# Kernel tuning notes

Measured on AMD Instinct MI355X. Metric: run time of the kernel, lower is better.

The kernel has to match this reference:

```python
import jax, jax.numpy as jnp
import numpy as np
import math

N, S, E, H = 4, 4096, 1024, 16
D = E // H  # head_dim = 64


def setup_inputs() -> dict:
    key = jax.random.key(0)
    ks = jax.random.split(key, 9)
    w = 1.0 / math.sqrt(E)
    mk = lambda k, shape: (jax.random.normal(k, shape, jnp.float32) * w)
    return {
        "x": jax.random.normal(ks[0], (N, S, E), jnp.float32),
        "Wq": mk(ks[1], (E, E)), "bq": mk(ks[2], (E,)),
        "Wk": mk(ks[3], (E, E)), "bk": mk(ks[4], (E,)),
        "Wv": mk(ks[5], (E, E)), "bv": mk(ks[6], (E,)),
        "Wo": mk(ks[7], (E, E)), "bo": mk(ks[8], (E,)),
    }


def reference(x, Wq, bq, Wk, bk, Wv, bv, Wo, bo):
    n, s, e = x.shape
    h, d = H, D
    scale = 1.0 / math.sqrt(d)

    def proj(W, b):
        # nn.Linear: x @ W.T + b, then view(N,S,H,D).transpose(1,2) -> (N,H,S,D)
        y = jnp.einsum('nse,fe->nsf', x, W) + b
        return y.reshape(n, s, h, d).transpose(0, 2, 1, 3)  # (N,H,S,D)

    Q = proj(Wq, bq)
    K = proj(Wk, bk)
    V = proj(Wv, bv)

    # Faithful reproduction of the source's einsum applied to ALREADY-transposed
    # (N,H,S,D) tensors: labels n,q,h,d bind to actual dims N,H,S,D, so the
    # result is (N, S, H, H) -- heads attending to heads at each position.
    scores = jnp.einsum('nqhd,nkhd->nhqk', Q, K) * scale  # (N,S,H,H)
    attn = jax.nn.softmax(scores, axis=-1)
    # Second einsum: attn labels n,h,q,l bind to N,S,H,H; V labels n,l,h,d bind
    # to N,H,S,D. Output nqhd has actual shape (N,H,S,D).
    out = jnp.einsum('nhql,nlhd->nqhd', attn, V)  # (N,H,S,D)
    out = out.reshape(n, s, e)  # scrambled flat reshape, as in the source
    return jnp.einsum('nse,fe->nsf', out, Wo) + bo
```

## Files before the change

kernel.cpp:

```cpp
#include <hip/hip_runtime.h>
#include <hip/hip_fp16.h>
#include <stddef.h>


typedef _Float16 f16_t;
typedef _Float16 f16x8 __attribute__((ext_vector_type(8)));
typedef _Float16 f16x4 __attribute__((ext_vector_type(4)));
typedef float    f32x4 __attribute__((ext_vector_type(4)));

static constexpr int Sdim = 4096;
static constexpr int Edim = 1024;
static constexpr int Mrows = 4 * Sdim;
static constexpr size_t MATEL = (size_t)Mrows * Edim;
static constexpr size_t WEL = (size_t)Edim * Edim;
static constexpr int BM = 128, BN = 128, BK = 32;
static constexpr int TILE = BM * BK;

__device__ __forceinline__ void gload_lds16(const f16_t* g, f16_t* l) {
  __builtin_amdgcn_global_load_lds(
      (const __attribute__((address_space(1))) void*)g,
      (__attribute__((address_space(3))) void*)l, 16, 0, 0);
}

__global__ __launch_bounds__(256) void cvt_kernel(
    const float* __restrict__ s0, const float* __restrict__ s1,
    const float* __restrict__ s2, const float* __restrict__ s3,
    const float* __restrict__ s4,
    f16_t* __restrict__ d0, f16_t* __restrict__ d1, f16_t* __restrict__ d2,
    f16_t* __restrict__ d3, f16_t* __restrict__ d4) {
  const float* s; f16_t* d; size_t nv;
  switch (blockIdx.y) {
    case 0: s = s0; d = d0; nv = MATEL / 4; break;
    case 1: s = s1; d = d1; nv = WEL / 4; break;
    case 2: s = s2; d = d2; nv = WEL / 4; break;
    case 3: s = s3; d = d3; nv = WEL / 4; break;
    default: s = s4; d = d4; nv = WEL / 4; break;
  }
  const size_t stride = (size_t)gridDim.x * 256;
  for (size_t i = blockIdx.x * 256 + threadIdx.x; i < nv; i += stride) {
    const f32x4 v = ((const f32x4*)s)[i];
    f16x4 h;
#pragma unroll
    for (int j = 0; j < 4; j++) h[j] = (f16_t)v[j];
    ((f16x4*)d)[i] = h;
  }
}

template <bool SCRA, typename TOut>
__device__ __forceinline__ void gemm_f16(const f16_t* __restrict__ A,
                                         const f16_t* __restrict__ B,
                                         const float* __restrict__ bias,
                                         TOut* __restrict__ C) {
  __shared__ __align__(16) f16_t As[TILE];
  __shared__ __align__(16) f16_t Bs[TILE];
  const int t = threadIdx.x;
  const int bm = blockIdx.x * BM;
  const int bn = blockIdx.y * BN;
  const int lane = t & 63;
  const int wave = t >> 6;
  const int wm = (wave >> 1) * 64;
  const int wn = (wave & 1) * 64;
  const int row16 = lane & 15;
  const int quad = lane >> 4;

  f32x4 acc[4][4] = {};

  const int lr = t >> 2;
  const int lc = (t & 3) * 8;
  f16_t* la = &As[t * 8];
  f16_t* lb = &Bs[t * 8];
  const f16_t* gb = B + (size_t)(bn + lr) * Edim + lc;

  for (int k0 = 0; k0 < Edim; k0 += BK) {
#pragma unroll
    for (int half = 0; half < 2; half++) {
      const f16_t* ga;
      if constexpr (SCRA) {
        const int R = bm + lr + half * 64;
        const int n = R >> 12, h = (R >> 8) & 15, shi = R & 255;
        const int c = k0 + lc;
        ga = A + ((size_t)((n << 12) + (shi << 4) + (c >> 6))) * Edim +
             (h << 6) + (c & 63);
      } else {
        ga = A + (size_t)(bm + lr + half * 64) * Edim + k0 + lc;
      }
      gload_lds16(ga, la + half * (64 * BK));
      gload_lds16(gb + k0 + half * (size_t)(64 * Edim), lb + half * (64 * BK));
    }
    __syncthreads();

    f16x8 af[4], bf[4];
#pragma unroll
    for (int i = 0; i < 4; i++)
      af[i] = *(const f16x8*)&As[(wm + i * 16 + row16) * BK + quad * 8];
#pragma unroll
    for (int j = 0; j < 4; j++)
      bf[j] = *(const f16x8*)&Bs[(wn + j * 16 + row16) * BK + quad * 8];
#pragma unroll
    for (int i = 0; i < 4; i++)
#pragma unroll
      for (int j = 0; j < 4; j++)
        acc[i][j] = __builtin_amdgcn_mfma_f32_16x16x32_f16(af[i], bf[j], acc[i][j], 0, 0, 0);
    __syncthreads();
  }

#pragma unroll
  for (int j = 0; j < 4; j++) {
    const int col = bn + wn + j * 16 + row16;
    const float bv = bias[col];
#pragma unroll
    for (int i = 0; i < 4; i++) {
      const int rb = bm + wm + i * 16 + quad * 4;
#pragma unroll
      for (int r = 0; r < 4; r++)
        C[(size_t)(rb + r) * Edim + col] = (TOut)(acc[i][j][r] + bv);
    }
  }
}

__global__ __launch_bounds__(256) void qkv_kernel(
    const f16_t* __restrict__ x,
    const f16_t* __restrict__ Wq, const float* __restrict__ bq,
    const f16_t* __restrict__ Wk, const float* __restrict__ bk,
    const f16_t* __restrict__ Wv, const float* __restrict__ bv,
    f16_t* __restrict__ Qb, f16_t* __restrict__ Kb, f16_t* __restrict__ Vb) {
  const f16_t* W; const float* bi; f16_t* C;
  if (blockIdx.z == 0)      { W = Wq; bi = bq; C = Qb; }
  else if (blockIdx.z == 1) { W = Wk; bi = bk; C = Kb; }
  else                      { W = Wv; bi = bv; C = Vb; }
  gemm_f16<false, f16_t>(x, W, bi, C);
}

__global__ __launch_bounds__(256) void outp_kernel(
    const f16_t* __restrict__ Ab, const f16_t* __restrict__ Wo,
    const float* __restrict__ bo, float* __restrict__ out) {
  gemm_f16<true, float>(Ab, Wo, bo, out);
}

__global__ __launch_bounds__(256) void attn_kernel(f16_t* __restrict__ Qb,
                                                   const f16_t* __restrict__ Kb,
                                                   const f16_t* __restrict__ Vb) {
  const int pos = blockIdx.x;
  __shared__ float q[16][65], k[16][65], v[16][65];
  __shared__ float p[16][17];
  const int t = threadIdx.x;
  f16_t* Qr = Qb + (size_t)pos * Edim;
  const f16_t* Kr = Kb + (size_t)pos * Edim;
  const f16_t* Vr = Vb + (size_t)pos * Edim;

  {
    const int h = t >> 4, d0 = (t & 15) * 4;
    const f16x4 qq = *(const f16x4*)(Qr + 4 * t);
    const f16x4 kk = *(const f16x4*)(Kr + 4 * t);
    const f16x4 vv = *(const f16x4*)(Vr + 4 * t);
#pragma unroll
    for (int j = 0; j < 4; j++) {
      q[h][d0 + j] = (float)qq[j];
      k[h][d0 + j] = (float)kk[j];
      v[h][d0 + j] = (float)vv[j];
    }
  }
  __syncthreads();
  {
    const int qh = t >> 4, kh = t & 15;
    float a = 0.f;
#pragma unroll
    for (int d = 0; d < 64; d++) a += q[qh][d] * k[kh][d];
    p[qh][kh] = a * 0.125f;
  }
  __syncthreads();
  if (t < 16) {
    float m = -1e30f;
#pragma unroll
    for (int kh = 0; kh < 16; kh++) m = fmaxf(m, p[t][kh]);
    float e[16], sum = 0.f;
#pragma unroll
    for (int kh = 0; kh < 16; kh++) { e[kh] = __expf(p[t][kh] - m); sum += e[kh]; }
    const float inv = 1.f / sum;
#pragma unroll
    for (int kh = 0; kh < 16; kh++) p[t][kh] = e[kh] * inv;
  }
  __syncthreads();
  {
    const int h = t >> 4, d0 = (t & 15) * 4;
    float o0 = 0.f, o1 = 0.f, o2 = 0.f, o3 = 0.f;
#pragma unroll
    for (int l = 0; l < 16; l++) {
      const float w = p[h][l];
      o0 += w * v[l][d0];
      o1 += w * v[l][d0 + 1];
      o2 += w * v[l][d0 + 2];
      o3 += w * v[l][d0 + 3];
    }
    f16x4 r;
    r[0] = (f16_t)o0; r[1] = (f16_t)o1; r[2] = (f16_t)o2; r[3] = (f16_t)o3;
    *(f16x4*)(Qr + 4 * t) = r;
  }
}

extern "C" void kernel_launch(void* const* d_in, const int* in_sizes, int n_in,
                              void* d_out, int out_size, void* d_ws, size_t ws_size,
                              hipStream_t stream) {
  const float* x  = (const float*)d_in[0];
  const float* Wq = (const float*)d_in[1];
  const float* bq = (const float*)d_in[2];
  const float* Wk = (const float*)d_in[3];
  const float* bk = (const float*)d_in[4];
  const float* Wv = (const float*)d_in[5];
  const float* bv = (const float*)d_in[6];
  const float* Wo = (const float*)d_in[7];
  const float* bo = (const float*)d_in[8];
  float* out = (float*)d_out;

  f16_t* xh  = (f16_t*)d_ws;
  f16_t* Wqh = xh + MATEL;
  f16_t* Wkh = Wqh + WEL;
  f16_t* Wvh = Wkh + WEL;
  f16_t* Woh = Wvh + WEL;
  f16_t* Qb  = Woh + WEL;
  f16_t* Kb  = Qb + MATEL;
  f16_t* Vb  = Kb + MATEL;

  const dim3 blk(256);
  cvt_kernel<<<dim3(2048, 5), blk, 0, stream>>>(x, Wq, Wk, Wv, Wo,
                                                xh, Wqh, Wkh, Wvh, Woh);
  qkv_kernel<<<dim3(Mrows / BM, Edim / BN, 3), blk, 0, stream>>>(
      xh, Wqh, bq, Wkh, bk, Wvh, bv, Qb, Kb, Vb);
  attn_kernel<<<dim3(Mrows), blk, 0, stream>>>(Qb, Kb, Vb);
  outp_kernel<<<dim3(Mrows / BM, Edim / BN), blk, 0, stream>>>(Qb, Woh, bo, out);
}
```

Baseline: 388.5 us.

## Use 32x32 MFMA with swizzled LDS and write scrambled attention output directly

The GEMM core moves from 16x16x32 to 32x32x16 MFMA tiles with an XOR-swizzled LDS layout, cutting LDS bank conflicts and fragment loads per MFMA. The attention kernel now writes its output in the scrambled row order into a separate buffer, so the output-projection GEMM reads A contiguously instead of computing scattered addresses. This costs an extra activation-sized workspace buffer and relies on the swizzle and scatter mapping being correct.

Result: no change. 393.7 us (+1.3%).

```diff
diff --git a/kernel.cpp b/kernel.cpp
--- a/kernel.cpp
+++ b/kernel.cpp
@@ -6,7 +6,8 @@
 typedef _Float16 f16_t;
 typedef _Float16 f16x8 __attribute__((ext_vector_type(8)));
 typedef _Float16 f16x4 __attribute__((ext_vector_type(4)));
-typedef float    f32x4 __attribute__((ext_vector_type(4)));
+typedef float    f32x4  __attribute__((ext_vector_type(4)));
+typedef float    f32x16 __attribute__((ext_vector_type(16)));
 
 static constexpr int Sdim = 4096;
 static constexpr int Edim = 1024;
@@ -46,7 +47,7 @@
   }
 }
 
-template <bool SCRA, typename TOut>
+template <typename TOut>
 __device__ __forceinline__ void gemm_f16(const f16_t* __restrict__ A,
                                          const f16_t* __restrict__ B,
                                          const float* __restrict__ bias,
@@ -60,60 +61,56 @@
   const int wave = t >> 6;
   const int wm = (wave >> 1) * 64;
   const int wn = (wave & 1) * 64;
-  const int row16 = lane & 15;
-  const int quad = lane >> 4;
-
-  f32x4 acc[4][4] = {};
+  const int r32 = lane & 31;
+  const int kgrp = lane >> 5;
+
+  f32x16 acc[2][2] = {};
 
   const int lr = t >> 2;
-  const int lc = (t & 3) * 8;
+  const int lc = ((t & 3) ^ (lr & 3)) * 8;
   f16_t* la = &As[t * 8];
   f16_t* lb = &Bs[t * 8];
-  const f16_t* gb = B + (size_t)(bn + lr) * Edim + lc;
+  const f16_t* gaBase = A + (size_t)(bm + lr) * Edim + lc;
+  const f16_t* gbBase = B + (size_t)(bn + lr) * Edim + lc;
 
   for (int k0 = 0; k0 < Edim; k0 += BK) {
-#pragma unroll
-    for (int half = 0; half < 2; half++) {
-      const f16_t* ga;
-      if constexpr (SCRA) {
-        const int R = bm + lr + half * 64;
-        const int n = R >> 12, h = (R >> 8) & 15, shi = R & 255;
-        const int c = k0 + lc;
-        ga = A + ((size_t)((n << 12) + (shi << 4) + (c >> 6))) * Edim +
-             (h << 6) + (c & 63);
-      } else {
-        ga = A + (size_t)(bm + lr + half * 64) * Edim + k0 + lc;
+    gload_lds16(gaBase + k0, la);
+    gload_lds16(gaBase + k0 + (size_t)64 * Edim, la + 64 * BK);
+    gload_lds16(gbBase + k0, lb);
+    gload_lds16(gbBase + k0 + (size_t)64 * Edim, lb + 64 * BK);
+    __syncthreads();
+
+#pragma unroll
+    for (int ks = 0; ks < 2; ks++) {
+      const int gidx = ((ks * 2 + kgrp) ^ (r32 & 3)) * 8;
+      f16x8 af[2], bf[2];
+#pragma unroll
+      for (int i = 0; i < 2; i++)
+        af[i] = *(const f16x8*)&As[(wm + i * 32 + r32) * BK + gidx];
+#pragma unroll
+      for (int j = 0; j < 2; j++)
+        bf[j] = *(const f16x8*)&Bs[(wn + j * 32 + r32) * BK + gidx];
+#pragma unroll
+      for (int i = 0; i < 2; i++)
+#pragma unroll
+        for (int j = 0; j < 2; j++)
+          acc[i][j] = __builtin_amdgcn_mfma_f32_32x32x16_f16(af[i], bf[j], acc[i][j], 0, 0, 0);
+    }
+    __syncthreads();
+  }
+
+#pragma unroll
+  for (int j = 0; j < 2; j++) {
+    const int col = bn + wn + j * 32 + r32;
+    const float bv = bias[col];
+#pragma unroll
+    for (int i = 0; i < 2; i++) {
+      const int rb = bm + wm + i * 32 + 4 * kgrp;
+#pragma unroll
+      for (int reg = 0; reg < 16; reg++) {
+        const int row = rb + (reg & 3) + 8 * (reg >> 2);
+        C[(size_t)row * Edim + col] = (TOut)(acc[i][j][reg] + bv);
       }
-      gload_lds16(ga, la + half * (64 * BK));
-      gload_lds16(gb + k0 + half * (size_t)(64 * Edim), lb + half * (64 * BK));
-    }
-    __syncthreads();
-
-    f16x8 af[4], bf[4];
-#pragma unroll
-    for (int i = 0; i < 4; i++)
-      af[i] = *(const f16x8*)&As[(wm + i * 16 + row16) * BK + quad * 8];
-#pragma unroll
-    for (int j = 0; j < 4; j++)
-      bf[j] = *(const f16x8*)&Bs[(wn + j * 16 + row16) * BK + quad * 8];
-#pragma unroll
-    for (int i = 0; i < 4; i++)
-#pragma unroll
-      for (int j = 0; j < 4; j++)
-        acc[i][j] = __builtin_amdgcn_mfma_f32_16x16x32_f16(af[i], bf[j], acc[i][j], 0, 0, 0);
-    __syncthreads();
-  }
-
-#pragma unroll
-  for (int j = 0; j < 4; j++) {
-    const int col = bn + wn + j * 16 + row16;
-    const float bv = bias[col];
-#pragma unroll
-    for (int i = 0; i < 4; i++) {
-      const int rb = bm + wm + i * 16 + quad * 4;
-#pragma unroll
-      for (int r = 0; r < 4; r++)
-        C[(size_t)(rb + r) * Edim + col] = (TOut)(acc[i][j][r] + bv);
     }
   }
 }
@@ -128,23 +125,24 @@
   if (blockIdx.z == 0)      { W = Wq; bi = bq; C = Qb; }
   else if (blockIdx.z == 1) { W = Wk; bi = bk; C = Kb; }
   else                      { W = Wv; bi = bv; C = Vb; }
-  gemm_f16<false, f16_t>(x, W, bi, C);
+  gemm_f16<f16_t>(x, W, bi, C);
 }
 
 __global__ __launch_bounds__(256) void outp_kernel(
     const f16_t* __restrict__ Ab, const f16_t* __restrict__ Wo,
     const float* __restrict__ bo, float* __restrict__ out) {
-  gemm_f16<true, float>(Ab, Wo, bo, out);
-}
-
-__global__ __launch_bounds__(256) void attn_kernel(f16_t* __restrict__ Qb,
+  gemm_f16<float>(Ab, Wo, bo, out);
+}
+
+__global__ __launch_bounds__(256) void attn_kernel(const f16_t* __restrict__ Qb,
                                                    const f16_t* __restrict__ Kb,
-                                                   const f16_t* __restrict__ Vb) {
+                                                   const f16_t* __restrict__ Vb,
+                                                   f16_t* __restrict__ Ab) {
   const int pos = blockIdx.x;
   __shared__ float q[16][65], k[16][65], v[16][65];
   __shared__ float p[16][17];
   const int t = threadIdx.x;
-  f16_t* Qr = Qb + (size_t)pos * Edim;
+  const f16_t* Qr = Qb + (size_t)pos * Edim;
   const f16_t* Kr = Kb + (size_t)pos * Edim;
   const f16_t* Vr = Vb + (size_t)pos * Edim;
 
@@ -194,7 +192,9 @@
     }
     f16x4 r;
     r[0] = (f16_t)o0; r[1] = (f16_t)o1; r[2] = (f16_t)o2; r[3] = (f16_t)o3;
-    *(f16x4*)(Qr + 4 * t) = r;
+    const int srow = ((pos >> 12) << 12) + (h << 8) + ((pos & 4095) >> 4);
+    const int scol = ((pos & 15) << 6) + d0;
+    *(f16x4*)(Ab + (size_t)srow * Edim + scol) = r;
   }
 }
 
@@ -220,12 +220,13 @@
   f16_t* Qb  = Woh + WEL;
   f16_t* Kb  = Qb + MATEL;
   f16_t* Vb  = Kb + MATEL;
+  f16_t* Ab  = Vb + MATEL;
 
   const dim3 blk(256);
   cvt_kernel<<<dim3(2048, 5), blk, 0, stream>>>(x, Wq, Wk, Wv, Wo,
                                                 xh, Wqh, Wkh, Wvh, Woh);
   qkv_kernel<<<dim3(Mrows / BM, Edim / BN, 3), blk, 0, stream>>>(
       xh, Wqh, bq, Wkh, bk, Wvh, bv, Qb, Kb, Vb);
-  attn_kernel<<<dim3(Mrows), blk, 0, stream>>>(Qb, Kb, Vb);
-  outp_kernel<<<dim3(Mrows / BM, Edim / BN), blk, 0, stream>>>(Qb, Woh, bo, out);
-}
+  attn_kernel<<<dim3(Mrows), blk, 0, stream>>>(Qb, Kb, Vb, Ab);
+  outp_kernel<<<dim3(Mrows / BM, Edim / BN), blk, 0, stream>>>(Ab, Woh, bo, out);
+}
```

## Use MFMA in per-position attention and write scrambled layout directly

Applied to the files above, without the earlier changes.

The head-to-head attention now runs one position per wavefront, four per block, and uses MFMA instructions for both the QK^T scores and the P·V product. Softmax is done in registers with cross-lane shuffles instead of shared-memory passes and extra barriers. The attention output goes to a separate buffer already in the scrambled layout, so the output projection GEMM can load A contiguously without per-row index arithmetic. The trade-offs are an extra workspace buffer, scattered 2-byte stores in the attention epilogue, and fp16 rounding of the softmax probabilities.

Result: faster. 348.2 us (-10.4%).

```diff
diff --git a/kernel.cpp b/kernel.cpp
--- a/kernel.cpp
+++ b/kernel.cpp
@@ -46,7 +46,7 @@
   }
 }
 
-template <bool SCRA, typename TOut>
+template <typename TOut>
 __device__ __forceinline__ void gemm_f16(const f16_t* __restrict__ A,
                                          const f16_t* __restrict__ B,
                                          const float* __restrict__ bias,
@@ -69,24 +69,14 @@
   const int lc = (t & 3) * 8;
   f16_t* la = &As[t * 8];
   f16_t* lb = &Bs[t * 8];
-  const f16_t* gb = B + (size_t)(bn + lr) * Edim + lc;
+  const f16_t* gaBase = A + (size_t)(bm + lr) * Edim + lc;
+  const f16_t* gbBase = B + (size_t)(bn + lr) * Edim + lc;
 
   for (int k0 = 0; k0 < Edim; k0 += BK) {
-#pragma unroll
-    for (int half = 0; half < 2; half++) {
-      const f16_t* ga;
-      if constexpr (SCRA) {
-        const int R = bm + lr + half * 64;
-        const int n = R >> 12, h = (R >> 8) & 15, shi = R & 255;
-        const int c = k0 + lc;
-        ga = A + ((size_t)((n << 12) + (shi << 4) + (c >> 6))) * Edim +
-             (h << 6) + (c & 63);
-      } else {
-        ga = A + (size_t)(bm + lr + half * 64) * Edim + k0 + lc;
-      }
-      gload_lds16(ga, la + half * (64 * BK));
-      gload_lds16(gb + k0 + half * (size_t)(64 * Edim), lb + half * (64 * BK));
-    }
+    gload_lds16(gaBase + k0, la);
+    gload_lds16(gaBase + k0 + (size_t)64 * Edim, la + 64 * BK);
+    gload_lds16(gbBase + k0, lb);
+    gload_lds16(gbBase + k0 + (size_t)64 * Edim, lb + 64 * BK);
     __syncthreads();
 
     f16x8 af[4], bf[4];
@@ -128,73 +118,81 @@
   if (blockIdx.z == 0)      { W = Wq; bi = bq; C = Qb; }
   else if (blockIdx.z == 1) { W = Wk; bi = bk; C = Kb; }
   else                      { W = Wv; bi = bv; C = Vb; }
-  gemm_f16<false, f16_t>(x, W, bi, C);
+  gemm_f16<f16_t>(x, W, bi, C);
 }
 
 __global__ __launch_bounds__(256) void outp_kernel(
     const f16_t* __restrict__ Ab, const f16_t* __restrict__ Wo,
     const float* __restrict__ bo, float* __restrict__ out) {
-  gemm_f16<true, float>(Ab, Wo, bo, out);
-}
-
-__global__ __launch_bounds__(256) void attn_kernel(f16_t* __restrict__ Qb,
+  gemm_f16<float>(Ab, Wo, bo, out);
+}
+
+__global__ __launch_bounds__(256) void attn_kernel(const f16_t* __restrict__ Qb,
                                                    const f16_t* __restrict__ Kb,
-                                                   const f16_t* __restrict__ Vb) {
-  const int pos = blockIdx.x;
-  __shared__ float q[16][65], k[16][65], v[16][65];
-  __shared__ float p[16][17];
+                                                   const f16_t* __restrict__ Vb,
+                                                   f16_t* __restrict__ Ab) {
+  __shared__ __align__(16) f16_t Vs[4][1024];
   const int t = threadIdx.x;
-  f16_t* Qr = Qb + (size_t)pos * Edim;
+  const int w = t >> 6;
+  const int lane = t & 63;
+  const int l16 = lane & 15;
+  const int quad = lane >> 4;
+  const int pos = blockIdx.x * 4 + w;
+  const int n4 = pos >> 12;
+  const int s = pos & (Sdim - 1);
+
+  const f16_t* Qr = Qb + (size_t)pos * Edim;
   const f16_t* Kr = Kb + (size_t)pos * Edim;
   const f16_t* Vr = Vb + (size_t)pos * Edim;
 
-  {
-    const int h = t >> 4, d0 = (t & 15) * 4;
-    const f16x4 qq = *(const f16x4*)(Qr + 4 * t);
-    const f16x4 kk = *(const f16x4*)(Kr + 4 * t);
-    const f16x4 vv = *(const f16x4*)(Vr + 4 * t);
-#pragma unroll
-    for (int j = 0; j < 4; j++) {
-      q[h][d0 + j] = (float)qq[j];
-      k[h][d0 + j] = (float)kk[j];
-      v[h][d0 + j] = (float)vv[j];
-    }
-  }
+  *(f16x8*)&Vs[w][lane * 16]     = *(const f16x8*)(Vr + lane * 16);
+  *(f16x8*)&Vs[w][lane * 16 + 8] = *(const f16x8*)(Vr + lane * 16 + 8);
+
+  f32x4 sacc = {};
+#pragma unroll
+  for (int step = 0; step < 2; step++) {
+    const int off = l16 * 64 + step * 32 + quad * 8;
+    const f16x8 kf = *(const f16x8*)(Kr + off);
+    const f16x8 qf = *(const f16x8*)(Qr + off);
+    sacc = __builtin_amdgcn_mfma_f32_16x16x32_f16(kf, qf, sacc, 0, 0, 0);
+  }
+#pragma unroll
+  for (int r = 0; r < 4; r++) sacc[r] *= 0.125f;
+
+  float m = fmaxf(fmaxf(sacc[0], sacc[1]), fmaxf(sacc[2], sacc[3]));
+  m = fmaxf(m, __shfl_xor(m, 16));
+  m = fmaxf(m, __shfl_xor(m, 32));
+  float e[4];
+#pragma unroll
+  for (int r = 0; r < 4; r++) e[r] = __expf(sacc[r] - m);
+  float l = (e[0] + e[1]) + (e[2] + e[3]);
+  l += __shfl_xor(l, 16);
+  l += __shfl_xor(l, 32);
+  const float inv = 1.0f / l;
+  f16x4 pa;
+#pragma unroll
+  for (int r = 0; r < 4; r++) pa[r] = (f16_t)(e[r] * inv);
+
   __syncthreads();
-  {
-    const int qh = t >> 4, kh = t & 15;
-    float a = 0.f;
-#pragma unroll
-    for (int d = 0; d < 64; d++) a += q[qh][d] * k[kh][d];
-    p[qh][kh] = a * 0.125f;
-  }
-  __syncthreads();
-  if (t < 16) {
-    float m = -1e30f;
-#pragma unroll
-    for (int kh = 0; kh < 16; kh++) m = fmaxf(m, p[t][kh]);
-    float e[16], sum = 0.f;
-#pragma unroll
-    for (int kh = 0; kh < 16; kh++) { e[kh] = __expf(p[t][kh] - m); sum += e[kh]; }
-    const float inv = 1.f / sum;
-#pragma unroll
-    for (int kh = 0; kh < 16; kh++) p[t][kh] = e[kh] * inv;
-  }
-  __syncthreads();
-  {
-    const int h = t >> 4, d0 = (t & 15) * 4;
-    float o0 = 0.f, o1 = 0.f, o2 = 0.f, o3 = 0.f;
-#pragma unroll
-    for (int l = 0; l < 16; l++) {
-      const float w = p[h][l];
-      o0 += w * v[l][d0];
-      o1 += w * v[l][d0 + 1];
-      o2 += w * v[l][d0 + 2];
-      o3 += w * v[l][d0 + 3];
-    }
-    f16x4 r;
-    r[0] = (f16_t)o0; r[1] = (f16_t)o1; r[2] = (f16_t)o2; r[3] = (f16_t)o3;
-    *(f16x4*)(Qr + 4 * t) = r;
+  f32x4 oacc[4];
+#pragma unroll
+  for (int dc = 0; dc < 4; dc++) {
+    f16x4 vbf;
+#pragma unroll
+    for (int j = 0; j < 4; j++)
+      vbf[j] = Vs[w][(quad * 4 + j) * 64 + dc * 16 + l16];
+    f32x4 z = {};
+    oacc[dc] = __builtin_amdgcn_mfma_f32_16x16x16f16(pa, vbf, z, 0, 0, 0);
+  }
+
+  const size_t obase =
+      ((size_t)(n4 << 12) + (size_t)(s >> 4)) * Edim + (size_t)(s & 15) * 64 + l16;
+#pragma unroll
+  for (int reg = 0; reg < 4; reg++) {
+    const size_t rowoff = obase + (size_t)(quad * 4 + reg) * 256 * Edim;
+#pragma unroll
+    for (int dc = 0; dc < 4; dc++)
+      Ab[rowoff + dc * 16] = (f16_t)oacc[dc][reg];
   }
 }
 
@@ -220,12 +218,13 @@
   f16_t* Qb  = Woh + WEL;
   f16_t* Kb  = Qb + MATEL;
   f16_t* Vb  = Kb + MATEL;
+  f16_t* Ab  = Vb + MATEL;
 
   const dim3 blk(256);
   cvt_kernel<<<dim3(2048, 5), blk, 0, stream>>>(x, Wq, Wk, Wv, Wo,
                                                 xh, Wqh, Wkh, Wvh, Woh);
   qkv_kernel<<<dim3(Mrows / BM, Edim / BN, 3), blk, 0, stream>>>(
       xh, Wqh, bq, Wkh, bk, Wvh, bv, Qb, Kb, Vb);
-  attn_kernel<<<dim3(Mrows), blk, 0, stream>>>(Qb, Kb, Vb);
-  outp_kernel<<<dim3(Mrows / BM, Edim / BN), blk, 0, stream>>>(Qb, Woh, bo, out);
-}
+  attn_kernel<<<dim3(Mrows / 4), blk, 0, stream>>>(Qb, Kb, Vb, Ab);
+  outp_kernel<<<dim3(Mrows / BM, Edim / BN), blk, 0, stream>>>(Ab, Woh, bo, out);
+}
```
